# Performance work log

Measured on AMD Instinct MI355X. Metric: run time of the kernel, lower is better.

Reference implementation:

```python
import jax, jax.numpy as jnp
import numpy as np

B, N = 32, 512
NB_TAU, NB_G, NB_W = 8, 8, 6
FLOOR = 0.001
SLOPE_RANGE = (0.5, 4.0)
BIAS_RANGE = (-2.0, 2.0)


def _basis(x, nb, kind):
    # MonotoneBasis: fixed grid of slopes/biases, monotone activation per basis.
    slopes = jnp.asarray(np.linspace(SLOPE_RANGE[0], SLOPE_RANGE[1], nb), x.dtype)
    biases = jnp.asarray(np.linspace(BIAS_RANGE[0], BIAS_RANGE[1], nb), x.dtype)
    z = x[..., None] * slopes + biases  # [..., nb]
    return jax.nn.softplus(z) if kind == 'softplus' else jax.nn.sigmoid(z)


def _normalize_scores(scores, mask, eps=1e-6):
    scores = jnp.where(mask, scores, 0.0)
    denom = jnp.clip(mask.sum(axis=1, keepdims=True), 1)
    mean = scores.sum(axis=1, keepdims=True) / denom
    scores = scores - mean
    var = (scores ** 2 * mask).sum(axis=1, keepdims=True) / denom
    return scores / jnp.sqrt(var + eps)


def setup_inputs() -> dict:
    key = jax.random.key(0)
    k1, k2, k3, k4, k5 = jax.random.split(key, 5)
    return {
        'predictions': jax.random.normal(k1, (B, N), dtype=jnp.float32),
        # targets in [0,1): all valid (no -1 padding), ties have measure zero
        'targets': jax.random.uniform(k2, (B, N), dtype=jnp.float32),
        'theta_tau': jax.random.normal(k3, (NB_TAU,), dtype=jnp.float32) * 0.1,
        'theta_g': jax.random.normal(k4, (NB_G,), dtype=jnp.float32) * 0.1,
        'theta_w': jax.random.normal(k5, (NB_W,), dtype=jnp.float32) * 0.1,
    }


def reference(predictions, targets, theta_tau, theta_g, theta_w):
    mask = ~jnp.isclose(targets, -1.0)
    s = _normalize_scores(predictions, mask)
    r = targets
    n = predictions.shape[1]
    iu, ju = np.triu_indices(n, k=1)  # static pair enumeration, P = n*(n-1)/2

    dr = r[:, iu] - r[:, ju]                      # [B, P]
    t = jnp.sign(dr)
    keep = (t != 0) & mask[:, iu] & mask[:, ju]   # drop ties / padded pairs
    ds = s[:, iu] - s[:, ju]
    abs_dr = jnp.abs(dr)

    # learned nonnegative combination coefficients (monotone outputs)
    c_tau = jax.nn.softplus(theta_tau)
    c_g = jax.nn.softplus(theta_g)
    c_w = jax.nn.softplus(theta_w)

    tau = _basis(abs_dr, NB_TAU, 'softplus') @ c_tau   # learned margin
    m = tau - t * ds
    g = _basis(m, NB_G, 'softplus') @ c_g              # learned penalty
    w = FLOOR + _basis(abs_dr, NB_W, 'sigmoid') @ c_w  # learned gap weight
    pair_loss = g * w

    kf = keep.astype(pair_loss.dtype)
    denom = jnp.clip(kf.sum(axis=1), 1.0)
    row_loss = (pair_loss * kf).sum(axis=1) / denom    # per-row mean over kept pairs
    valid_row = (kf.sum(axis=1) > 0).astype(pair_loss.dtype)
    return (row_loss * valid_row).sum() / jnp.clip(valid_row.sum(), 1.0)
```

## Files before the change

kernel.cpp:

```cpp
#include <hip/hip_runtime.h>
#include <math.h>

#define BB 32
#define NN 512
#define PP 130816
#define PSPLIT 130560
#define KBLK 32
#define TW 1024
#define TG 2048

#define OFF_S   0
#define OFF_TW  16384
#define OFF_TG  18440
#define OFF_GB  20496
#define OFF_RS  20512
#define OFF_RC  20544
#define OFF_CNT 20576

__device__ __forceinline__ float splus(float z) {
    return fmaxf(z, 0.0f) + __logf(1.0f + __expf(-fabsf(z)));
}

__device__ __constant__ float ST8[8] = {0.5f, 1.0f, 1.5f, 2.0f, 2.5f, 3.0f, 3.5f, 4.0f};
__device__ __constant__ float BT8[8] = {
    (float)(-2.0), (float)(-2.0 + 4.0/7.0), (float)(-2.0 + 8.0/7.0),
    (float)(-2.0 + 12.0/7.0), (float)(-2.0 + 16.0/7.0),
    (float)(-2.0 + 20.0/7.0), (float)(-2.0 + 24.0/7.0), 2.0f };
__device__ __constant__ float SW6[6] = {0.5f, (float)(0.5 + 3.5/5.0), (float)(0.5 + 7.0/5.0),
    (float)(0.5 + 10.5/5.0), (float)(0.5 + 14.0/5.0), 4.0f};
__device__ __constant__ float BW6[6] = {-2.0f, (float)(-2.0 + 4.0/5.0), (float)(-2.0 + 8.0/5.0),
    (float)(-2.0 + 12.0/5.0), (float)(-2.0 + 16.0/5.0), 2.0f};

__global__ __launch_bounds__(256)
void prep_kernel(const float* __restrict__ pred, const float* __restrict__ targ,
                 const float* __restrict__ th_tau, const float* __restrict__ th_g,
                 const float* __restrict__ th_w, float* __restrict__ ws)
{
    const int bid = blockIdx.x, tid = threadIdx.x;
    if (bid < BB) {
        const int base = bid * NN;
        float x0 = pred[base + tid], x1 = pred[base + tid + 256];
        float t0 = targ[base + tid], t1 = targ[base + tid + 256];
        float m0 = (fabsf(t0 + 1.0f) > 1.00001e-5f) ? 1.0f : 0.0f;
        float m1 = (fabsf(t1 + 1.0f) > 1.00001e-5f) ? 1.0f : 0.0f;
        float xs0 = x0 * m0, xs1 = x1 * m1;
        float lsum = xs0 + xs1;
        float lsq  = xs0 * xs0 + xs1 * xs1;
        float lcnt = m0 + m1;
        #pragma unroll
        for (int off = 32; off; off >>= 1) {
            lsum += __shfl_down(lsum, off);
            lsq  += __shfl_down(lsq,  off);
            lcnt += __shfl_down(lcnt, off);
        }
        __shared__ float red[3][4];
        const int lane = tid & 63, wv = tid >> 6;
        if (lane == 0) { red[0][wv] = lsum; red[1][wv] = lsq; red[2][wv] = lcnt; }
        __syncthreads();
        __shared__ float mean_s, rsig_s;
        if (tid == 0) {
            float S = 0.0f, Q = 0.0f, C = 0.0f;
            for (int i = 0; i < 4; i++) { S += red[0][i]; Q += red[1][i]; C += red[2][i]; }
            float denom = fmaxf(C, 1.0f);
            float mean = S / denom;
            float var = Q / denom - mean * mean;
            mean_s = mean;
            rsig_s = 1.0f / sqrtf(var + 1e-6f);
            ws[OFF_RS + bid] = 0.0f;
            ws[OFF_RC + bid] = 0.0f;
        }
        __syncthreads();
        ws[OFF_S + base + tid]       = (xs0 - mean_s) * rsig_s;
        ws[OFF_S + base + tid + 256] = (xs1 - mean_s) * rsig_s;
    } else if (bid < BB + 4) {
        const int e = (bid - BB) * 256 + tid;
        float adr = (float)e * (1.0f / (float)(TW - 1));
        float tau = 0.0f, w = 0.001f;
        #pragma unroll
        for (int k = 0; k < 8; k++)
            tau = fmaf(splus(fmaf(adr, ST8[k], BT8[k])), splus(th_tau[k]), tau);
        #pragma unroll
        for (int k = 0; k < 6; k++) {
            float z = fmaf(adr, SW6[k], BW6[k]);
            w = fmaf(1.0f / (1.0f + __expf(-z)), splus(th_w[k]), w);
        }
        float2* g_tw = (float2*)(ws + OFF_TW);
        g_tw[e] = make_float2(tau, w);
        if (e == TW - 1) g_tw[TW] = make_float2(tau, w);
        if (bid == BB && tid == 0) *((unsigned int*)(ws + OFF_CNT)) = 0u;
    } else {
        const int e = (bid - BB - 4) * 256 + tid;
        float m = fmaf((float)e, 32.0f / (float)(TG - 1), -16.0f);
        float g = 0.0f;
        #pragma unroll
        for (int k = 0; k < 8; k++)
            g = fmaf(splus(fmaf(m, ST8[k], BT8[k])), splus(th_g[k]), g);
        ws[OFF_TG + e] = g;
        if (e == TG - 1) ws[OFF_TG + TG] = g;
        if (bid == BB + 4 && tid == 0) {
            float gB = 0.0f;
            for (int k = 0; k < 8; k++) gB += splus(th_g[k]) * ST8[k];
            ws[OFF_GB] = gB;
        }
    }
}

__global__ __launch_bounds__(256)
void pair_kernel(const float* __restrict__ targ, float* __restrict__ ws,
                 float* __restrict__ out)
{
    const int b   = blockIdx.x & (BB - 1);
    const int sub = blockIdx.x >> 5;
    const int tid = threadIdx.x;
    __shared__ float2 sRS[NN];
    __shared__ float2 sTW[TW + 1];
    __shared__ float  sTG[TG + 1];
    __shared__ bool   sLast;

    const float* s_all = ws + OFF_S;
    const float2* g_tw = (const float2*)(ws + OFF_TW);
    #pragma unroll
    for (int e = tid; e < NN; e += 256)
        sRS[e] = make_float2(targ[b * NN + e], s_all[b * NN + e]);
    for (int e = tid; e < TW + 1; e += 256) sTW[e] = g_tw[e];
    for (int e = tid; e < TG + 1; e += 256) sTG[e] = ws[OFF_TG + e];
    const float gB = ws[OFF_GB];
    __syncthreads();

    float lsum = 0.0f, lcnt = 0.0f;
    for (int p = sub * 256 + tid; p < PP; p += KBLK * 256) {
        int d, x;
        if (p < PSPLIT) { d = (p >> 9) + 1; x = p & (NN - 1); }
        else            { d = NN / 2;       x = p - PSPLIT;   }
        const int j = (x + d) & (NN - 1);
        float2 rsi = sRS[x];
        float2 rsj = sRS[j];
        float dr  = rsi.x - rsj.x;
        float adr = fabsf(dr);
        float ds  = rsi.y - rsj.y;
        float tds = (dr > 0.0f) ? ds : -ds;
        float u  = adr * (float)(TW - 1);
        float kf = floorf(u);
        float fr = u - kf;
        int   k  = (int)kf;
        float2 tw0 = sTW[k], tw1 = sTW[k + 1];
        float tau = fmaf(fr, tw1.x - tw0.x, tw0.x);
        float w   = fmaf(fr, tw1.y - tw0.y, tw0.y);
        float m  = tau - tds;
        float um = fminf(fmaxf(m, -16.0f), 16.0f);
        float u2 = fmaf(um, (float)(TG - 1) * (1.0f / 32.0f), (float)(TG - 1) * 0.5f);
        float kf2 = floorf(u2);
        float fr2 = u2 - kf2;
        int   k2  = (int)kf2;
        float g0 = sTG[k2], g1 = sTG[k2 + 1];
        float g  = fmaf(fr2, g1 - g0, g0);
        g = fmaf(fmaxf(m - 16.0f, 0.0f), gB, g);
        if (dr != 0.0f) { lsum = fmaf(g, w, lsum); lcnt += 1.0f; }
    }
    #pragma unroll
    for (int off = 32; off; off >>= 1) {
        lsum += __shfl_down(lsum, off);
        lcnt += __shfl_down(lcnt, off);
    }
    __shared__ float red[2][4];
    const int lane = tid & 63, wv = tid >> 6;
    if (lane == 0) { red[0][wv] = lsum; red[1][wv] = lcnt; }
    __syncthreads();
    float* rowsum = ws + OFF_RS;
    float* rowcnt = ws + OFF_RC;
    if (tid == 0) {
        float S = red[0][0] + red[0][1] + red[0][2] + red[0][3];
        float C = red[1][0] + red[1][1] + red[1][2] + red[1][3];
        atomicAdd(&rowsum[b], S);
        atomicAdd(&rowcnt[b], C);
        __threadfence();
        unsigned int prev = atomicAdd((unsigned int*)(ws + OFF_CNT), 1u);
        sLast = (prev == (unsigned int)(BB * KBLK - 1));
    }
    __syncthreads();
    if (sLast && tid < 64) {
        float val = 0.0f, vld = 0.0f;
        if (tid < BB) {
            float s = atomicAdd(&rowsum[tid], 0.0f);
            float c = atomicAdd(&rowcnt[tid], 0.0f);
            float rl = s / fmaxf(c, 1.0f);
            float v  = (c > 0.0f) ? 1.0f : 0.0f;
            val = rl * v;
            vld = v;
        }
        #pragma unroll
        for (int off = 32; off; off >>= 1) {
            val += __shfl_down(val, off);
            vld += __shfl_down(vld, off);
        }
        if (tid == 0) out[0] = val / fmaxf(vld, 1.0f);
    }
}

extern "C" void kernel_launch(void* const* d_in, const int* in_sizes, int n_in,
                              void* d_out, int out_size, void* d_ws, size_t ws_size,
                              hipStream_t stream) {
    const float* pred   = (const float*)d_in[0];
    const float* targ   = (const float*)d_in[1];
    const float* th_tau = (const float*)d_in[2];
    const float* th_g   = (const float*)d_in[3];
    const float* th_w   = (const float*)d_in[4];
    float* ws  = (float*)d_ws;
    float* out = (float*)d_out;

    prep_kernel<<<BB + 12, 256, 0, stream>>>(pred, targ, th_tau, th_g, th_w, ws);
    pair_kernel<<<BB * KBLK, 256, 0, stream>>>(targ, ws, out);
}
```

Baseline: 90.17 us.

## Pack g-table as float2 pairs, halve its size, move finalization to separate kernel

The g lookup table is halved to 1024 entries and stored as (g[k], g[k+1]) float2 pairs, so each pair needs one LDS read instead of two for the interpolation. The last-block atomic counter, threadfence and serialized final reduction in pair_kernel are replaced by a tiny third kernel that reads the row sums. Prep launches fewer blocks. The trade-offs are one more kernel launch and coarser interpolation of g, which may reduce accuracy.

Result: faster. 83.31 us (-7.6%).

```diff
diff --git a/kernel.cpp b/kernel.cpp
--- a/kernel.cpp
+++ b/kernel.cpp
@@ -7,15 +7,14 @@
 #define PSPLIT 130560
 #define KBLK 32
 #define TW 1024
-#define TG 2048
+#define TG 1024
 
 #define OFF_S   0
 #define OFF_TW  16384
-#define OFF_TG  18440
-#define OFF_GB  20496
-#define OFF_RS  20512
-#define OFF_RC  20544
-#define OFF_CNT 20576
+#define OFF_TG  18436
+#define OFF_RS  20488
+#define OFF_RC  20520
+#define OFF_GB  20552
 
 __device__ __forceinline__ float splus(float z) {
     return fmaxf(z, 0.0f) + __logf(1.0f + __expf(-fabsf(z)));
@@ -30,6 +29,14 @@
     (float)(0.5 + 10.5/5.0), (float)(0.5 + 14.0/5.0), 4.0f};
 __device__ __constant__ float BW6[6] = {-2.0f, (float)(-2.0 + 4.0/5.0), (float)(-2.0 + 8.0/5.0),
     (float)(-2.0 + 12.0/5.0), (float)(-2.0 + 16.0/5.0), 2.0f};
+
+__device__ __forceinline__ float g_of_m(float m, const float* th_g) {
+    float g = 0.0f;
+    #pragma unroll
+    for (int k = 0; k < 8; k++)
+        g = fmaf(splus(fmaf(m, ST8[k], BT8[k])), splus(th_g[k]), g);
+    return g;
+}
 
 __global__ __launch_bounds__(256)
 void prep_kernel(const float* __restrict__ pred, const float* __restrict__ targ,
@@ -87,18 +94,17 @@
         float2* g_tw = (float2*)(ws + OFF_TW);
         g_tw[e] = make_float2(tau, w);
         if (e == TW - 1) g_tw[TW] = make_float2(tau, w);
-        if (bid == BB && tid == 0) *((unsigned int*)(ws + OFF_CNT)) = 0u;
     } else {
         const int e = (bid - BB - 4) * 256 + tid;
-        float m = fmaf((float)e, 32.0f / (float)(TG - 1), -16.0f);
-        float g = 0.0f;
-        #pragma unroll
-        for (int k = 0; k < 8; k++)
-            g = fmaf(splus(fmaf(m, ST8[k], BT8[k])), splus(th_g[k]), g);
-        ws[OFF_TG + e] = g;
-        if (e == TG - 1) ws[OFF_TG + TG] = g;
-        if (bid == BB + 4 && tid == 0) {
+        const float step = 32.0f / (float)(TG - 1);
+        float m0v = fmaf((float)e, step, -16.0f);
+        float ga = g_of_m(m0v, th_g);
+        float gb = (e < TG - 1) ? g_of_m(m0v + step, th_g) : ga;
+        float2* g_gp = (float2*)(ws + OFF_TG);
+        g_gp[e] = make_float2(ga, gb);
+        if (e == 0) {
             float gB = 0.0f;
+            #pragma unroll
             for (int k = 0; k < 8; k++) gB += splus(th_g[k]) * ST8[k];
             ws[OFF_GB] = gB;
         }
@@ -106,24 +112,23 @@
 }
 
 __global__ __launch_bounds__(256)
-void pair_kernel(const float* __restrict__ targ, float* __restrict__ ws,
-                 float* __restrict__ out)
+void pair_kernel(const float* __restrict__ targ, float* __restrict__ ws)
 {
     const int b   = blockIdx.x & (BB - 1);
     const int sub = blockIdx.x >> 5;
     const int tid = threadIdx.x;
     __shared__ float2 sRS[NN];
     __shared__ float2 sTW[TW + 1];
-    __shared__ float  sTG[TG + 1];
-    __shared__ bool   sLast;
+    __shared__ float2 sTG[TG];
 
     const float* s_all = ws + OFF_S;
     const float2* g_tw = (const float2*)(ws + OFF_TW);
+    const float2* g_gp = (const float2*)(ws + OFF_TG);
     #pragma unroll
     for (int e = tid; e < NN; e += 256)
         sRS[e] = make_float2(targ[b * NN + e], s_all[b * NN + e]);
     for (int e = tid; e < TW + 1; e += 256) sTW[e] = g_tw[e];
-    for (int e = tid; e < TG + 1; e += 256) sTG[e] = ws[OFF_TG + e];
+    for (int e = tid; e < TG; e += 256)     sTG[e] = g_gp[e];
     const float gB = ws[OFF_GB];
     __syncthreads();
 
@@ -146,14 +151,13 @@
         float2 tw0 = sTW[k], tw1 = sTW[k + 1];
         float tau = fmaf(fr, tw1.x - tw0.x, tw0.x);
         float w   = fmaf(fr, tw1.y - tw0.y, tw0.y);
-        float m  = tau - tds;
-        float um = fminf(fmaxf(m, -16.0f), 16.0f);
-        float u2 = fmaf(um, (float)(TG - 1) * (1.0f / 32.0f), (float)(TG - 1) * 0.5f);
+        float m   = tau - tds;
+        float um  = fminf(fmaxf(m, -16.0f), 16.0f);
+        float u2  = fmaf(um, (float)(TG - 1) * (1.0f / 32.0f), (float)(TG - 1) * 0.5f);
         float kf2 = floorf(u2);
         float fr2 = u2 - kf2;
-        int   k2  = (int)kf2;
-        float g0 = sTG[k2], g1 = sTG[k2 + 1];
-        float g  = fmaf(fr2, g1 - g0, g0);
+        float2 gp = sTG[(int)kf2];
+        float g   = fmaf(fr2, gp.y - gp.x, gp.x);
         g = fmaf(fmaxf(m - 16.0f, 0.0f), gB, g);
         if (dr != 0.0f) { lsum = fmaf(g, w, lsum); lcnt += 1.0f; }
     }
@@ -166,35 +170,31 @@
     const int lane = tid & 63, wv = tid >> 6;
     if (lane == 0) { red[0][wv] = lsum; red[1][wv] = lcnt; }
     __syncthreads();
-    float* rowsum = ws + OFF_RS;
-    float* rowcnt = ws + OFF_RC;
     if (tid == 0) {
         float S = red[0][0] + red[0][1] + red[0][2] + red[0][3];
         float C = red[1][0] + red[1][1] + red[1][2] + red[1][3];
-        atomicAdd(&rowsum[b], S);
-        atomicAdd(&rowcnt[b], C);
-        __threadfence();
-        unsigned int prev = atomicAdd((unsigned int*)(ws + OFF_CNT), 1u);
-        sLast = (prev == (unsigned int)(BB * KBLK - 1));
-    }
-    __syncthreads();
-    if (sLast && tid < 64) {
-        float val = 0.0f, vld = 0.0f;
-        if (tid < BB) {
-            float s = atomicAdd(&rowsum[tid], 0.0f);
-            float c = atomicAdd(&rowcnt[tid], 0.0f);
-            float rl = s / fmaxf(c, 1.0f);
-            float v  = (c > 0.0f) ? 1.0f : 0.0f;
-            val = rl * v;
-            vld = v;
-        }
-        #pragma unroll
-        for (int off = 32; off; off >>= 1) {
-            val += __shfl_down(val, off);
-            vld += __shfl_down(vld, off);
-        }
-        if (tid == 0) out[0] = val / fmaxf(vld, 1.0f);
-    }
+        atomicAdd(ws + OFF_RS + b, S);
+        atomicAdd(ws + OFF_RC + b, C);
+    }
+}
+
+__global__ void final_kernel(const float* __restrict__ ws, float* __restrict__ out)
+{
+    const int tid = threadIdx.x;
+    float val = 0.0f, vld = 0.0f;
+    if (tid < BB) {
+        float c = ws[OFF_RC + tid], s = ws[OFF_RS + tid];
+        float rl = s / fmaxf(c, 1.0f);
+        float v  = (c > 0.0f) ? 1.0f : 0.0f;
+        val = rl * v;
+        vld = v;
+    }
+    #pragma unroll
+    for (int off = 32; off; off >>= 1) {
+        val += __shfl_down(val, off);
+        vld += __shfl_down(vld, off);
+    }
+    if (tid == 0) out[0] = val / fmaxf(vld, 1.0f);
 }
 
 extern "C" void kernel_launch(void* const* d_in, const int* in_sizes, int n_in,
@@ -208,6 +208,7 @@
     float* ws  = (float*)d_ws;
     float* out = (float*)d_out;
 
-    prep_kernel<<<BB + 12, 256, 0, stream>>>(pred, targ, th_tau, th_g, th_w, ws);
-    pair_kernel<<<BB * KBLK, 256, 0, stream>>>(targ, ws, out);
-}
+    prep_kernel<<<BB + 8, 256, 0, stream>>>(pred, targ, th_tau, th_g, th_w, ws);
+    pair_kernel<<<BB * KBLK, 256, 0, stream>>>(targ, ws);
+    final_kernel<<<1, 64, 0, stream>>>(ws, out);
+}
```
